# Optimization experiments

Hardware: AMD Instinct MI355X
Metric: run time of the kernel (lower is better)

## Reference

```python
import jax, jax.numpy as jnp
import numpy as np

B, N = 4, 512
C_IN, RES, SR = 256, 7, 2
FC_DIM = 1024
NUM_CLASSES, BOX_DIM, BINS = 3, 6, 12
OUT_CH = NUM_CLASSES * (1 + BOX_DIM + 2 * BINS) + 1  # 94
IMG = 512
STRIDES = (8, 16, 32)


def setup_inputs() -> dict:
    key = jax.random.key(0)
    ks = jax.random.split(key, 12)
    feat_p3 = jax.random.normal(ks[0], (B, C_IN, IMG // 8, IMG // 8), jnp.float32)
    feat_p4 = jax.random.normal(ks[1], (B, C_IN, IMG // 16, IMG // 16), jnp.float32)
    feat_p5 = jax.random.normal(ks[2], (B, C_IN, IMG // 32, IMG // 32), jnp.float32)
    cy = jax.random.uniform(ks[3], (B, N), minval=64.0, maxval=448.0)
    cx = jax.random.uniform(ks[4], (B, N), minval=64.0, maxval=448.0)
    h = jax.random.uniform(ks[5], (B, N), minval=16.0, maxval=120.0)
    w = jax.random.uniform(ks[6], (B, N), minval=16.0, maxval=120.0)
    bbox2d = jnp.stack([cy - h / 2, cx - w / 2, cy + h / 2, cx + w / 2], -1)  # tlbr
    anchors = jnp.stack([cy, cx, h, w], -1)  # (y, x, l, w)
    anchor_id = jax.random.randint(ks[7], (B, N), 0, 9, dtype=jnp.int32)
    flat = C_IN * RES * RES
    fc1_w = jax.random.normal(ks[8], (FC_DIM, flat), jnp.float32) * 0.01
    fc1_b = jnp.zeros((FC_DIM,), jnp.float32)
    bn1_g = jnp.ones((FC_DIM,), jnp.float32)
    bn1_b = jnp.zeros((FC_DIM,), jnp.float32)
    fc2_w = jax.random.normal(ks[9], (FC_DIM, FC_DIM), jnp.float32) * 0.02
    fc2_b = jnp.zeros((FC_DIM,), jnp.float32)
    bn2_g = jnp.ones((FC_DIM,), jnp.float32)
    bn2_b = jnp.zeros((FC_DIM,), jnp.float32)
    pred_w = jax.random.normal(ks[10], (OUT_CH, FC_DIM), jnp.float32) * 0.02
    pred_b = jnp.zeros((OUT_CH,), jnp.float32)
    return dict(feat_p3=feat_p3, feat_p4=feat_p4, feat_p5=feat_p5, bbox2d=bbox2d,
                anchors=anchors, anchor_id=anchor_id, fc1_w=fc1_w, fc1_b=fc1_b,
                bn1_g=bn1_g, bn1_b=bn1_b, fc2_w=fc2_w, fc2_b=fc2_b,
                bn2_g=bn2_g, bn2_b=bn2_b, pred_w=pred_w, pred_b=pred_b)


def _roi_align(feat, boxes, scale):
    # feat: [C,H,W]; boxes: [N,4] tlbr in image coords; aligned=True ROIAlign.
    C, H, W = feat.shape
    S = RES * SR
    t = boxes[:, 0] * scale - 0.5
    l = boxes[:, 1] * scale - 0.5
    bh = (boxes[:, 2] - boxes[:, 0]) * scale / RES  # bin height
    bw = (boxes[:, 3] - boxes[:, 1]) * scale / RES
    g = (jnp.arange(S, dtype=feat.dtype) + 0.5) / SR  # sample offsets in bin units
    ys = t[:, None] + g[None, :] * bh[:, None]  # [N,S]
    xs = l[:, None] + g[None, :] * bw[:, None]
    yc = jnp.clip(ys, 0.0, H - 1.0)
    xc = jnp.clip(xs, 0.0, W - 1.0)
    y0 = jnp.floor(yc)
    x0 = jnp.floor(xc)
    y0i = y0.astype(jnp.int32)
    x0i = x0.astype(jnp.int32)
    y1i = jnp.minimum(y0i + 1, H - 1)
    x1i = jnp.minimum(x0i + 1, W - 1)
    ly = yc - y0
    lx = xc - x0

    def gat(yi, xi):  # -> [C,N,S,S]
        return feat[:, yi[:, :, None], xi[:, None, :]]

    w00 = ((1 - ly)[:, :, None] * (1 - lx)[:, None, :])[None]
    w01 = ((1 - ly)[:, :, None] * lx[:, None, :])[None]
    w10 = (ly[:, :, None] * (1 - lx)[:, None, :])[None]
    w11 = (ly[:, :, None] * lx[:, None, :])[None]
    v = gat(y0i, x0i) * w00 + gat(y0i, x1i) * w01 + gat(y1i, x0i) * w10 + gat(y1i, x1i) * w11
    v = jnp.transpose(v, (1, 0, 2, 3)).reshape(-1, C, RES, SR, RES, SR)
    return v.mean((3, 5))  # [N,C,RES,RES] avg over sampling grid


def _bn_train(x, g, b):
    m = x.mean(0)
    v = x.var(0)
    return (x - m) * jax.lax.rsqrt(v + 1e-5) * g + b


def _forward(feat_p3, feat_p4, feat_p5, bbox2d, anchors, fc1_w, fc1_b, bn1_g, bn1_b,
             fc2_w, fc2_b, bn2_g, bn2_b, pred_w, pred_b, anchor_id):
    feats = (feat_p3, feat_p4, feat_p5)
    lvl = anchor_id // 3  # [B,N] feature-level assignment
    # box_pooler: pool every box at every level, then select its assigned level
    # (equivalent to the torch gather/sort/cat dispatch, in original box order).
    sel = 0.0
    for i, s in enumerate(STRIDES):
        pooled = jax.vmap(lambda f, bx, sc=1.0 / s: _roi_align(f, bx, sc))(feats[i], bbox2d)
        sel = sel + pooled * (lvl == i)[..., None, None, None].astype(pooled.dtype)
    x = sel.reshape(B * N, -1)  # [B*N, C*7*7]
    x = jax.nn.relu(_bn_train(x @ fc1_w.T + fc1_b, bn1_g, bn1_b))
    x = jax.nn.relu(_bn_train(x @ fc2_w.T + fc2_b, bn2_g, bn2_b))
    pred = (x @ pred_w.T + pred_b).reshape(B, N, OUT_CH)
    # decode: slice per-loss channels then apply box deltas per category
    c0 = NUM_CLASSES + 1
    cat = pred[..., :c0]  # [B,N,4]
    b1 = c0 + NUM_CLASSES * BOX_DIM
    bbox3d = pred[..., c0:b1].reshape(B, N, NUM_CLASSES, BOX_DIM)
    yaw_cls = pred[..., b1:b1 + NUM_CLASSES * BINS]
    yaw_res = pred[..., b1 + NUM_CLASSES * BINS:]
    delta = bbox3d[..., :4]  # yxlw deltas per category
    zh = bbox3d[..., 4:]
    stride_px = jnp.exp2(lvl.astype(pred.dtype) + 3.0)  # 8/16/32
    yx = anchors[:, :, None, :2] + delta[..., :2] * stride_px[..., None, None]
    lw = anchors[:, :, None, 2:] * jnp.exp(jnp.clip(delta[..., 2:], -4.0, 4.0))
    box_out = jnp.concatenate([yx, lw, zh], -1).reshape(B, N, NUM_CLASSES * BOX_DIM)
    return jnp.concatenate([cat, box_out, yaw_cls, yaw_res], -1)  # [B,N,94]


def reference(feat_p3, feat_p4, feat_p5, bbox2d, anchors, anchor_id, fc1_w, fc1_b,
              bn1_g, bn1_b, fc2_w, fc2_b, bn2_g, bn2_b, pred_w, pred_b):
    return _forward(feat_p3, feat_p4, feat_p5, bbox2d, anchors, fc1_w, fc1_b, bn1_g,
                    bn1_b, fc2_w, fc2_b, bn2_g, bn2_b, pred_w, pred_b, anchor_id)
```

## Files before the change

kernel.cpp:

```cpp
#include <hip/hip_runtime.h>
#include <hip/hip_bf16.h>

typedef __attribute__((ext_vector_type(8))) short short8;
typedef __attribute__((ext_vector_type(4))) float floatx4;
typedef __attribute__((ext_vector_type(4))) unsigned short ushort4v;

#define DEVI __device__ __forceinline__


DEVI unsigned short f2bf(float v) {
  union { __hip_bfloat16 h; unsigned short u; } cv;
  cv.h = __float2bfloat16(v);
  return cv.u;
}
DEVI short f2bfs(float v) { return (short)f2bf(v); }

DEVI void gload16(const void* gptr, void* lptr) {
  __builtin_amdgcn_global_load_lds(
      (const __attribute__((address_space(1))) unsigned int*)gptr,
      (__attribute__((address_space(3))) unsigned int*)(unsigned long long)(uintptr_t)lptr,
      16, 0, 0);
}

__global__ void cvt_bf16x4_kernel(const float4* __restrict__ src,
                                  ushort4v* __restrict__ dst, size_t n4) {
  size_t i = (size_t)blockIdx.x * blockDim.x + threadIdx.x;
  if (i >= n4) return;
  float4 v = src[i];
  ushort4v o;
  o[0] = f2bf(v.x); o[1] = f2bf(v.y); o[2] = f2bf(v.z); o[3] = f2bf(v.w);
  dst[i] = o;
}

__global__ void cvt_pad_pred_kernel(const float* __restrict__ src,
                                    unsigned short* __restrict__ dst) {
  int i = blockIdx.x * blockDim.x + threadIdx.x;
  if (i >= 96 * 1024) return;
  int row = i >> 10;
  dst[i] = (row < 94) ? f2bf(src[i]) : (unsigned short)0;
}

__global__ __launch_bounds__(256) void wgen_kernel(
    const float* __restrict__ bbox, const int* __restrict__ aid,
    unsigned short* __restrict__ Wbuf, int2* __restrict__ rbase) {
  const int box = blockIdx.x;
  const int tid = threadIdx.x;
  __shared__ int sy0[14], sx0[14];
  __shared__ float sly[14], slx[14];
  __shared__ float wy[7][16], wx[7][16];

  const int lvl = aid[box] / 3;
  const int H = 64 >> lvl;
  const float scale = 0.125f / (float)(1 << lvl);

  if (tid < 28) {
    int s = tid;
    bool isY = s < 14;
    int k = isY ? s : s - 14;
    float lo = bbox[box * 4 + (isY ? 0 : 1)];
    float hi = bbox[box * 4 + (isY ? 2 : 3)];
    float t = lo * scale - 0.5f;
    float cell = (hi - lo) * scale * (1.0f / 7.0f);
    float pos = t + ((float)k + 0.5f) * 0.5f * cell;
    pos = fminf(fmaxf(pos, 0.0f), (float)(H - 1));
    int i0 = (int)floorf(pos);
    if (i0 > H - 2) i0 = H - 2;
    float fr = pos - (float)i0;
    if (isY) { sy0[k] = i0; sly[k] = fr; }
    else     { sx0[k] = i0; slx[k] = fr; }
  }
  __syncthreads();

  const int ryb = min(sy0[0], H - 16);
  const int rxb = min(sx0[0], H - 16);
  if (tid == 0) rbase[box] = make_int2(ryb, rxb);

  if (tid < 224) {
    int j = tid;
    bool isY = j < 112;
    int k2 = isY ? j : j - 112;
    int py = k2 >> 4, r = k2 & 15;
    int o0 = isY ? ryb : rxb;
    float acc = 0.f;
#pragma unroll
    for (int ss = 0; ss < 2; ++ss) {
      int s = 2 * py + ss;
      int rel = (isY ? sy0[s] : sx0[s]) - o0;
      float fr = isY ? sly[s] : slx[s];
      if (r == rel)     acc += 1.0f - fr;
      if (r == rel + 1) acc += fr;
    }
    if (isY) wy[py][r] = acc * 0.5f;
    else     wx[py][r] = acc * 0.5f;
  }
  __syncthreads();

  unsigned short* wb = Wbuf + (size_t)box * 13312;
  for (int idx = tid; idx < 49 * 256; idx += 256) {
    int cell = idx >> 8, k = idx & 255;
    int r = k >> 4, c = k & 15;
    int py = (cell * 37) >> 8;
    int px = cell - py * 7;
    wb[cell * 264 + k] = f2bf(wy[py][r] * wx[px][c]);
  }
}

__global__ __launch_bounds__(256) void roi_mm_kernel(
    const float* __restrict__ p3, const float* __restrict__ p4,
    const float* __restrict__ p5, const unsigned short* __restrict__ Wbuf,
    const int2* __restrict__ rbase, const int* __restrict__ aid,
    unsigned short* __restrict__ X) {
  constexpr int PS = 260;
  constexpr int WS = 264;
  __shared__ float P[32 * PS];
  __shared__ unsigned short W[64 * WS];

  const int box = blockIdx.x;
  const int oct = blockIdx.y;
  const int b = box >> 9;
  const int tid = threadIdx.x;
  const int lane = tid & 63, wid = tid >> 6;

  const int lvl = aid[box] / 3;
  const int H = 64 >> lvl;
  const int HH = H * H;
  const float* base = (lvl == 0) ? p3 : ((lvl == 1) ? p4 : p5);
  const int2 rb = rbase[box];
  const float* fb = base + ((size_t)b * 256 + oct * 32) * HH + rb.x * H + rb.y;

  const unsigned short* wsrc = Wbuf + (size_t)box * 13312;
  for (int s = tid; s < 1664; s += 256)
    gload16(wsrc + s * 8, (unsigned short*)W + s * 8);

  {
    const int r = lane >> 2, c4 = (lane & 3) * 4;
    const float* src0 = fb + r * H + c4;
#pragma unroll
    for (int it = 0; it < 8; ++it) {
      int ch = it * 4 + wid;
      gload16(src0 + (size_t)ch * HH, &P[ch * PS] + lane * 4);
    }
  }
  __syncthreads();

  const int fr = lane & 15, fg = lane >> 4;
  const int chf = wid >> 1;
  const int cellb = (wid & 1) * 32;

  floatx4 acc0 = (floatx4){0.f, 0.f, 0.f, 0.f};
  floatx4 acc1 = (floatx4){0.f, 0.f, 0.f, 0.f};

#pragma unroll
  for (int kk = 0; kk < 8; ++kk) {
    const float* ap = &P[(chf * 16 + fr) * PS + kk * 32 + fg * 8];
    floatx4 a0 = *(const floatx4*)ap;
    floatx4 a1 = *(const floatx4*)(ap + 4);
    short8 af;
    af[0] = f2bfs(a0[0]); af[1] = f2bfs(a0[1]); af[2] = f2bfs(a0[2]); af[3] = f2bfs(a0[3]);
    af[4] = f2bfs(a1[0]); af[5] = f2bfs(a1[1]); af[6] = f2bfs(a1[2]); af[7] = f2bfs(a1[3]);
    short8 b0 = *(const short8*)&W[(cellb + fr) * WS + kk * 32 + fg * 8];
    short8 b1 = *(const short8*)&W[(cellb + 16 + fr) * WS + kk * 32 + fg * 8];
    acc0 = __builtin_amdgcn_mfma_f32_16x16x32_bf16(af, b0, acc0, 0, 0, 0);
    acc1 = __builtin_amdgcn_mfma_f32_16x16x32_bf16(af, b1, acc1, 0, 0, 0);
  }

  unsigned short* xb = X + (size_t)box * 12544 + (size_t)(oct * 32 + chf * 16) * 49;
  {
    int cell = cellb + fr;
    if (cell < 49) {
#pragma unroll
      for (int q = 0; q < 4; ++q)
        xb[(fg * 4 + q) * 49 + cell] = f2bf(acc0[q]);
    }
    cell = cellb + 16 + fr;
    if (cell < 49) {
#pragma unroll
      for (int q = 0; q < 4; ++q)
        xb[(fg * 4 + q) * 49 + cell] = f2bf(acc1[q]);
    }
  }
}

template <int KSPLIT>
__global__ __launch_bounds__(256) void gemm_bt_swz(
    const unsigned short* __restrict__ A, const unsigned short* __restrict__ Bw,
    float* __restrict__ C, int M, int N, int K) {
  constexpr int BM = 128, BN = 128, BK = 64;
  __shared__ unsigned short As[BM * BK];
  __shared__ unsigned short Bs[BN * BK];

  const int tid = threadIdx.x;
  const int lane = tid & 63, wid = tid >> 6;
  const int wr = wid >> 1, wc = wid & 1;
  const int tm = blockIdx.x * BM, tn = blockIdx.y * BN;
  const int fr = lane & 15, fg = lane >> 4;

  const int kLen = K / KSPLIT;
  const int kTiles = kLen / BK;
  const int kBeg = blockIdx.z * kLen;
  float* Cz = C + (size_t)blockIdx.z * M * N;

  floatx4 acc[4][4];
#pragma unroll
  for (int i = 0; i < 4; ++i)
#pragma unroll
    for (int j = 0; j < 4; ++j)
      acc[i][j] = (floatx4){0.f, 0.f, 0.f, 0.f};

  for (int t = 0; t < kTiles; ++t) {
    const int k0 = kBeg + t * BK;
#pragma unroll
    for (int s = tid; s < BM * 8; s += 256) {
      int row = s >> 3, sl = s & 7;
      int slg = sl ^ (row & 7);
      gload16(&A[(size_t)(tm + row) * K + k0 + slg * 8], &As[s * 8]);
    }
#pragma unroll
    for (int s = tid; s < BN * 8; s += 256) {
      int row = s >> 3, sl = s & 7;
      int slg = sl ^ (row & 7);
      gload16(&Bw[(size_t)(tn + row) * K + k0 + slg * 8], &Bs[s * 8]);
    }
    __syncthreads();

#pragma unroll
    for (int kk = 0; kk < 2; ++kk) {
      short8 af[4], bf[4];
#pragma unroll
      for (int i = 0; i < 4; ++i) {
        int row = wr * 64 + i * 16 + fr;
        int sl = (kk * 4 + fg) ^ (row & 7);
        af[i] = *reinterpret_cast<const short8*>(&As[(row * 8 + sl) * 8]);
      }
#pragma unroll
      for (int j = 0; j < 4; ++j) {
        int row = wc * 64 + j * 16 + fr;
        int sl = (kk * 4 + fg) ^ (row & 7);
        bf[j] = *reinterpret_cast<const short8*>(&Bs[(row * 8 + sl) * 8]);
      }
#pragma unroll
      for (int i = 0; i < 4; ++i)
#pragma unroll
        for (int j = 0; j < 4; ++j)
          acc[i][j] = __builtin_amdgcn_mfma_f32_16x16x32_bf16(af[i], bf[j], acc[i][j], 0, 0, 0);
    }
    __syncthreads();
  }

#pragma unroll
  for (int i = 0; i < 4; ++i)
#pragma unroll
    for (int j = 0; j < 4; ++j)
#pragma unroll
      for (int q = 0; q < 4; ++q) {
        int rr = tm + wr * 64 + i * 16 + fg * 4 + q;
        int cc = tn + wc * 64 + j * 16 + fr;
        Cz[(size_t)rr * N + cc] = acc[i][j][q];
      }
}

template <int BM, int BN, int WAVES_M, int WAVES_N, int KSPLIT>
__global__ __launch_bounds__(256) void gemm_bt_kernel(
    const unsigned short* __restrict__ A, const unsigned short* __restrict__ Bw,
    float* __restrict__ C, int M, int N, int K) {
  constexpr int BK = 32;
  constexpr int WM = BM / WAVES_M, WN = BN / WAVES_N;
  constexpr int AF = WM / 16, BF = WN / 16;
  constexpr int ASLOT = BM * 4;
  constexpr int BSLOT = BN * 4;
  __shared__ unsigned short As[BM * BK];
  __shared__ unsigned short Bs[BN * BK];

  const int tid = threadIdx.x;
  const int lane = tid & 63, wid = tid >> 6;
  const int wr = wid / WAVES_N, wc = wid % WAVES_N;
  const int tm = blockIdx.x * BM, tn = blockIdx.y * BN;
  const int fr = lane & 15, fg = lane >> 4;

  const int kLen = K / KSPLIT;
  const int kBeg = blockIdx.z * kLen;
  float* Cz = C + (size_t)blockIdx.z * M * N;

  floatx4 acc[AF][BF];
#pragma unroll
  for (int i = 0; i < AF; ++i)
#pragma unroll
    for (int j = 0; j < BF; ++j)
      acc[i][j] = (floatx4){0.f, 0.f, 0.f, 0.f};

  for (int k0 = kBeg; k0 < kBeg + kLen; k0 += BK) {
#pragma unroll
    for (int s = tid; s < ASLOT; s += 256) {
      int row = s >> 2, kb = (s & 3) << 3;
      gload16(&A[(size_t)(tm + row) * K + k0 + kb], &As[s * 8]);
    }
#pragma unroll
    for (int s = tid; s < BSLOT; s += 256) {
      int row = s >> 2, kb = (s & 3) << 3;
      gload16(&Bw[(size_t)(tn + row) * K + k0 + kb], &Bs[s * 8]);
    }
    __syncthreads();

    short8 af[AF], bfv[BF];
#pragma unroll
    for (int i = 0; i < AF; ++i)
      af[i] = *reinterpret_cast<const short8*>(&As[(wr * WM + i * 16 + fr) * BK + fg * 8]);
#pragma unroll
    for (int j = 0; j < BF; ++j)
      bfv[j] = *reinterpret_cast<const short8*>(&Bs[(wc * WN + j * 16 + fr) * BK + fg * 8]);
#pragma unroll
    for (int i = 0; i < AF; ++i)
#pragma unroll
      for (int j = 0; j < BF; ++j)
        acc[i][j] = __builtin_amdgcn_mfma_f32_16x16x32_bf16(af[i], bfv[j], acc[i][j], 0, 0, 0);
    __syncthreads();
  }

#pragma unroll
  for (int i = 0; i < AF; ++i)
#pragma unroll
    for (int j = 0; j < BF; ++j)
#pragma unroll
      for (int q = 0; q < 4; ++q) {
        int rr = tm + wr * WM + i * 16 + fg * 4 + q;
        int cc = tn + wc * WN + j * 16 + fr;
        Cz[(size_t)rr * N + cc] = acc[i][j][q];
      }
}

__global__ void bn_stats_red_kernel(const float* __restrict__ Yp, float* __restrict__ Yred,
                                    float* __restrict__ psum, float* __restrict__ psq,
                                    int Ncols, int rowsPer, int P, size_t pstride) {
  int c = blockIdx.x * blockDim.x + threadIdx.x;
  int r0 = blockIdx.y * rowsPer;
  float s = 0.f, ss = 0.f;
  for (int r = 0; r < rowsPer; ++r) {
    size_t idx = (size_t)(r0 + r) * Ncols + c;
    float v = Yp[idx];
    for (int p = 1; p < P; ++p) v += Yp[idx + (size_t)p * pstride];
    Yred[idx] = v;
    s += v;
    ss += v * v;
  }
  psum[(size_t)blockIdx.y * Ncols + c] = s;
  psq[(size_t)blockIdx.y * Ncols + c] = ss;
}

__global__ void bn_finalize_kernel(const float* __restrict__ psum, const float* __restrict__ psq,
                                   const float* __restrict__ g, const float* __restrict__ b,
                                   float* __restrict__ scale, float* __restrict__ shift,
                                   int Ncols, int P, float invM) {
  int c = blockIdx.x * blockDim.x + threadIdx.x;
  if (c >= Ncols) return;
  float s = 0.f, ss = 0.f;
  for (int p = 0; p < P; ++p) {
    s += psum[(size_t)p * Ncols + c];
    ss += psq[(size_t)p * Ncols + c];
  }
  float mean = s * invM;
  float var = ss * invM - mean * mean;
  float rstd = rsqrtf(var + 1e-5f);
  float sc = rstd * g[c];
  scale[c] = sc;
  shift[c] = b[c] - mean * sc;
}

__global__ void bn_apply4_kernel(const float4* __restrict__ Y, const float* __restrict__ scale,
                                 const float* __restrict__ shift, ushort4v* __restrict__ X,
                                 int colGroupsMask, int total4) {
  int i = blockIdx.x * blockDim.x + threadIdx.x;
  if (i >= total4) return;
  int c0 = (i & colGroupsMask) * 4;
  float4 v = Y[i];
  ushort4v o;
  o[0] = f2bf(fmaxf(v.x * scale[c0 + 0] + shift[c0 + 0], 0.0f));
  o[1] = f2bf(fmaxf(v.y * scale[c0 + 1] + shift[c0 + 1], 0.0f));
  o[2] = f2bf(fmaxf(v.z * scale[c0 + 2] + shift[c0 + 2], 0.0f));
  o[3] = f2bf(fmaxf(v.w * scale[c0 + 3] + shift[c0 + 3], 0.0f));
  X[i] = o;
}

__global__ void decode_kernel(const float* __restrict__ Y3, const float* __restrict__ pb,
                              const float* __restrict__ anchors, const int* __restrict__ aid,
                              float* __restrict__ out) {
  int i = blockIdx.x * blockDim.x + threadIdx.x;
  if (i >= 2048 * 94) return;
  int bn = i / 94;
  int ch = i - bn * 94;
  size_t idx = (size_t)bn * 96 + ch;
  float v = Y3[idx] + Y3[idx + 2048 * 96] + Y3[idx + 2 * 2048 * 96] + Y3[idx + 3 * 2048 * 96];
  v += pb[ch];
  float o = v;
  if (ch >= 4 && ch < 22) {
    int q = ch - 4;
    int d = q % 6;
    if (d < 2) {
      float stride_px = (float)(8 << (aid[bn] / 3));
      o = anchors[(size_t)bn * 4 + d] + v * stride_px;
    } else if (d < 4) {
      float cl = fminf(fmaxf(v, -4.0f), 4.0f);
      o = anchors[(size_t)bn * 4 + d] * expf(cl);
    }
  }
  out[i] = o;
}

extern "C" void kernel_launch(void* const* d_in, const int* in_sizes, int n_in,
                              void* d_out, int out_size, void* d_ws, size_t ws_size,
                              hipStream_t stream) {
  const float* feat_p3   = (const float*)d_in[0];
  const float* feat_p4   = (const float*)d_in[1];
  const float* feat_p5   = (const float*)d_in[2];
  const float* bbox2d    = (const float*)d_in[3];
  const float* anchors   = (const float*)d_in[4];
  const int*   anchor_id = (const int*)d_in[5];
  const float* fc1_w     = (const float*)d_in[6];
  const float* bn1_g     = (const float*)d_in[8];
  const float* bn1_b     = (const float*)d_in[9];
  const float* fc2_w     = (const float*)d_in[10];
  const float* bn2_g     = (const float*)d_in[12];
  const float* bn2_b     = (const float*)d_in[13];
  const float* pred_w    = (const float*)d_in[14];
  const float* pred_b    = (const float*)d_in[15];
  float* out = (float*)d_out;

  const int M = 2048;
  const int K1 = 12544;
  const int FC = 1024;
  const int RG = 128;

  char* ws = (char*)d_ws;
  auto alloc = [&](size_t bytes) -> char* {
    char* p = ws;
    ws += (bytes + 255) & ~(size_t)255;
    return p;
  };
  unsigned short* W1b  = (unsigned short*)alloc((size_t)FC * K1 * 2);
  unsigned short* W2b  = (unsigned short*)alloc((size_t)FC * FC * 2);
  unsigned short* W3b  = (unsigned short*)alloc((size_t)96 * FC * 2);
  unsigned short* X1   = (unsigned short*)alloc((size_t)M * K1 * 2);
  unsigned short* Wbuf = (unsigned short*)alloc((size_t)M * 13312 * 2);
  int2*           rbas = (int2*)alloc((size_t)M * 8);
  float*          Yp   = (float*)alloc((size_t)4 * M * FC * 4);
  float*          Yr   = (float*)alloc((size_t)M * FC * 4);
  unsigned short* X2   = (unsigned short*)alloc((size_t)M * FC * 2);
  unsigned short* X3   = (unsigned short*)alloc((size_t)M * FC * 2);
  float*          Y3   = (float*)alloc((size_t)4 * M * 96 * 4);
  float*          ps   = (float*)alloc((size_t)RG * FC * 4);
  float*          pq   = (float*)alloc((size_t)RG * FC * 4);
  float*          sc1  = (float*)alloc((size_t)FC * 4);
  float*          sh1  = (float*)alloc((size_t)FC * 4);
  float*          sc2  = (float*)alloc((size_t)FC * 4);
  float*          sh2  = (float*)alloc((size_t)FC * 4);

  {
    size_t n4 = (size_t)FC * K1 / 4;
    cvt_bf16x4_kernel<<<(unsigned)((n4 + 255) / 256), 256, 0, stream>>>(
        (const float4*)fc1_w, (ushort4v*)W1b, n4);
  }
  {
    size_t n4 = (size_t)FC * FC / 4;
    cvt_bf16x4_kernel<<<(unsigned)((n4 + 255) / 256), 256, 0, stream>>>(
        (const float4*)fc2_w, (ushort4v*)W2b, n4);
  }
  cvt_pad_pred_kernel<<<(96 * 1024) / 256, 256, 0, stream>>>(pred_w, W3b);

  wgen_kernel<<<2048, 256, 0, stream>>>(bbox2d, anchor_id, Wbuf, rbas);
  roi_mm_kernel<<<dim3(2048, 8), 256, 0, stream>>>(feat_p3, feat_p4, feat_p5,
                                                   Wbuf, rbas, anchor_id, X1);

  gemm_bt_swz<4><<<dim3(M / 128, FC / 128, 4), 256, 0, stream>>>(X1, W1b, Yp, M, FC, K1);

  bn_stats_red_kernel<<<dim3(FC / 256, RG), 256, 0, stream>>>(Yp, Yr, ps, pq, FC, M / RG, 4, (size_t)M * FC);
  bn_finalize_kernel<<<FC / 256, 256, 0, stream>>>(ps, pq, bn1_g, bn1_b, sc1, sh1, FC, RG, 1.0f / M);
  bn_apply4_kernel<<<(M * FC / 4) / 256, 256, 0, stream>>>(
      (const float4*)Yr, sc1, sh1, (ushort4v*)X2, FC / 4 - 1, M * FC / 4);

  gemm_bt_swz<2><<<dim3(M / 128, FC / 128, 2), 256, 0, stream>>>(X2, W2b, Yp, M, FC, FC);

  bn_stats_red_kernel<<<dim3(FC / 256, RG), 256, 0, stream>>>(Yp, Yr, ps, pq, FC, M / RG, 2, (size_t)M * FC);
  bn_finalize_kernel<<<FC / 256, 256, 0, stream>>>(ps, pq, bn2_g, bn2_b, sc2, sh2, FC, RG, 1.0f / M);
  bn_apply4_kernel<<<(M * FC / 4) / 256, 256, 0, stream>>>(
      (const float4*)Yr, sc2, sh2, (ushort4v*)X3, FC / 4 - 1, M * FC / 4);

  gemm_bt_kernel<64, 96, 2, 2, 4><<<dim3(M / 64, 1, 4), 256, 0, stream>>>(X3, W3b, Y3, M, 96, FC);

  decode_kernel<<<(2048 * 94 + 255) / 256, 256, 0, stream>>>(Y3, pred_b, anchors, anchor_id, out);
}
```

Measured before the change: 303.5 us.

## Fuse ROI weight generation into the ROI-align MFMA kernel

Removes the separate kernel that materialized dense bf16 bilinear weight matrices per box in global memory. Each ROI block now computes separable y/x weights into shared memory and forms the B-operand on the fly as wy*wx products before the MFMA. This avoids writing and re-reading a large weight buffer and one launch, at the cost of recomputing the small weight setup per channel-octave block and extra ALU work in the inner loop.

```diff
diff --git a/kernel.cpp b/kernel.cpp
--- a/kernel.cpp
+++ b/kernel.cpp
@@ -40,17 +40,26 @@
   dst[i] = (row < 94) ? f2bf(src[i]) : (unsigned short)0;
 }
 
-__global__ __launch_bounds__(256) void wgen_kernel(
-    const float* __restrict__ bbox, const int* __restrict__ aid,
-    unsigned short* __restrict__ Wbuf, int2* __restrict__ rbase) {
-  const int box = blockIdx.x;
-  const int tid = threadIdx.x;
+__global__ __launch_bounds__(256) void roi_mm2_kernel(
+    const float* __restrict__ p3, const float* __restrict__ p4,
+    const float* __restrict__ p5, const float* __restrict__ bbox,
+    const int* __restrict__ aid, unsigned short* __restrict__ X) {
+  constexpr int PS = 260;
+  __shared__ float P[32 * PS];
+  __shared__ float wyx[238];
   __shared__ int sy0[14], sx0[14];
   __shared__ float sly[14], slx[14];
-  __shared__ float wy[7][16], wx[7][16];
+
+  const int box = blockIdx.x;
+  const int oct = blockIdx.y;
+  const int b = box >> 9;
+  const int tid = threadIdx.x;
+  const int lane = tid & 63, wid = tid >> 6;
 
   const int lvl = aid[box] / 3;
   const int H = 64 >> lvl;
+  const int HH = H * H;
+  const float* base = (lvl == 0) ? p3 : ((lvl == 1) ? p4 : p5);
   const float scale = 0.125f / (float)(1 << lvl);
 
   if (tid < 28) {
@@ -73,7 +82,7 @@
 
   const int ryb = min(sy0[0], H - 16);
   const int rxb = min(sx0[0], H - 16);
-  if (tid == 0) rbase[box] = make_int2(ryb, rxb);
+  const float* fb = base + ((size_t)b * 256 + oct * 32) * HH + ryb * H + rxb;
 
   if (tid < 224) {
     int j = tid;
@@ -90,47 +99,8 @@
       if (r == rel)     acc += 1.0f - fr;
       if (r == rel + 1) acc += fr;
     }
-    if (isY) wy[py][r] = acc * 0.5f;
-    else     wx[py][r] = acc * 0.5f;
-  }
-  __syncthreads();
-
-  unsigned short* wb = Wbuf + (size_t)box * 13312;
-  for (int idx = tid; idx < 49 * 256; idx += 256) {
-    int cell = idx >> 8, k = idx & 255;
-    int r = k >> 4, c = k & 15;
-    int py = (cell * 37) >> 8;
-    int px = cell - py * 7;
-    wb[cell * 264 + k] = f2bf(wy[py][r] * wx[px][c]);
-  }
-}
-
-__global__ __launch_bounds__(256) void roi_mm_kernel(
-    const float* __restrict__ p3, const float* __restrict__ p4,
-    const float* __restrict__ p5, const unsigned short* __restrict__ Wbuf,
-    const int2* __restrict__ rbase, const int* __restrict__ aid,
-    unsigned short* __restrict__ X) {
-  constexpr int PS = 260;
-  constexpr int WS = 264;
-  __shared__ float P[32 * PS];
-  __shared__ unsigned short W[64 * WS];
-
-  const int box = blockIdx.x;
-  const int oct = blockIdx.y;
-  const int b = box >> 9;
-  const int tid = threadIdx.x;
-  const int lane = tid & 63, wid = tid >> 6;
-
-  const int lvl = aid[box] / 3;
-  const int H = 64 >> lvl;
-  const int HH = H * H;
-  const float* base = (lvl == 0) ? p3 : ((lvl == 1) ? p4 : p5);
-  const int2 rb = rbase[box];
-  const float* fb = base + ((size_t)b * 256 + oct * 32) * HH + rb.x * H + rb.y;
-
-  const unsigned short* wsrc = Wbuf + (size_t)box * 13312;
-  for (int s = tid; s < 1664; s += 256)
-    gload16(wsrc + s * 8, (unsigned short*)W + s * 8);
+    wyx[(isY ? 0 : 119) + py * 17 + r] = acc * 0.5f;
+  }
 
   {
     const int r = lane >> 2, c4 = (lane & 3) * 4;
@@ -146,6 +116,12 @@
   const int fr = lane & 15, fg = lane >> 4;
   const int chf = wid >> 1;
   const int cellb = (wid & 1) * 32;
+  const int cell0 = cellb + fr;
+  const int cell1 = cellb + 16 + fr;
+  const int py0 = (cell0 * 37) >> 8, px0 = cell0 - py0 * 7;
+  const int py1 = (cell1 * 37) >> 8, px1 = cell1 - py1 * 7;
+  const float* wyB = wyx;
+  const float* wxB = wyx + 119;
 
   floatx4 acc0 = (floatx4){0.f, 0.f, 0.f, 0.f};
   floatx4 acc1 = (floatx4){0.f, 0.f, 0.f, 0.f};
@@ -158,26 +134,31 @@
     short8 af;
     af[0] = f2bfs(a0[0]); af[1] = f2bfs(a0[1]); af[2] = f2bfs(a0[2]); af[3] = f2bfs(a0[3]);
     af[4] = f2bfs(a1[0]); af[5] = f2bfs(a1[1]); af[6] = f2bfs(a1[2]); af[7] = f2bfs(a1[3]);
-    short8 b0 = *(const short8*)&W[(cellb + fr) * WS + kk * 32 + fg * 8];
-    short8 b1 = *(const short8*)&W[(cellb + 16 + fr) * WS + kk * 32 + fg * 8];
+
+    const int r = 2 * kk + (fg >> 1);
+    const int c0 = (fg & 1) * 8;
+    const float w0 = wyB[py0 * 17 + r];
+    const float w1 = wyB[py1 * 17 + r];
+    const float* x0 = &wxB[px0 * 17 + c0];
+    const float* x1 = &wxB[px1 * 17 + c0];
+    short8 b0, b1;
+#pragma unroll
+    for (int e = 0; e < 8; ++e) {
+      b0[e] = f2bfs(w0 * x0[e]);
+      b1[e] = f2bfs(w1 * x1[e]);
+    }
     acc0 = __builtin_amdgcn_mfma_f32_16x16x32_bf16(af, b0, acc0, 0, 0, 0);
     acc1 = __builtin_amdgcn_mfma_f32_16x16x32_bf16(af, b1, acc1, 0, 0, 0);
   }
 
   unsigned short* xb = X + (size_t)box * 12544 + (size_t)(oct * 32 + chf * 16) * 49;
-  {
-    int cell = cellb + fr;
-    if (cell < 49) {
-#pragma unroll
-      for (int q = 0; q < 4; ++q)
-        xb[(fg * 4 + q) * 49 + cell] = f2bf(acc0[q]);
-    }
-    cell = cellb + 16 + fr;
-    if (cell < 49) {
-#pragma unroll
-      for (int q = 0; q < 4; ++q)
-        xb[(fg * 4 + q) * 49 + cell] = f2bf(acc1[q]);
-    }
+#pragma unroll
+  for (int q = 0; q < 4; ++q)
+    xb[(fg * 4 + q) * 49 + cell0] = f2bf(acc0[q]);
+  if (cell1 < 49) {
+#pragma unroll
+    for (int q = 0; q < 4; ++q)
+      xb[(fg * 4 + q) * 49 + cell1] = f2bf(acc1[q]);
   }
 }
 
@@ -439,8 +420,6 @@
   unsigned short* W2b  = (unsigned short*)alloc((size_t)FC * FC * 2);
   unsigned short* W3b  = (unsigned short*)alloc((size_t)96 * FC * 2);
   unsigned short* X1   = (unsigned short*)alloc((size_t)M * K1 * 2);
-  unsigned short* Wbuf = (unsigned short*)alloc((size_t)M * 13312 * 2);
-  int2*           rbas = (int2*)alloc((size_t)M * 8);
   float*          Yp   = (float*)alloc((size_t)4 * M * FC * 4);
   float*          Yr   = (float*)alloc((size_t)M * FC * 4);
   unsigned short* X2   = (unsigned short*)alloc((size_t)M * FC * 2);
@@ -465,9 +444,8 @@
   }
   cvt_pad_pred_kernel<<<(96 * 1024) / 256, 256, 0, stream>>>(pred_w, W3b);
 
-  wgen_kernel<<<2048, 256, 0, stream>>>(bbox2d, anchor_id, Wbuf, rbas);
-  roi_mm_kernel<<<dim3(2048, 8), 256, 0, stream>>>(feat_p3, feat_p4, feat_p5,
-                                                   Wbuf, rbas, anchor_id, X1);
+  roi_mm2_kernel<<<dim3(2048, 8), 256, 0, stream>>>(feat_p3, feat_p4, feat_p5,
+                                                    bbox2d, anchor_id, X1);
 
   gemm_bt_swz<4><<<dim3(M / 128, FC / 128, 4), 256, 0, stream>>>(X1, W1b, Yp, M, FC, K1);
 
```

Result: faster. 256.5 us (-15.5%).
